# Kernel optimization log

Measured on AMD Instinct MI355X. Metric: run time of the kernel, lower is better.

Reference implementation:

```python
import jax, jax.numpy as jnp
import numpy as np

N_NODES = 100000
N_EDGES = 1600000
IN_NODE = 64
IN_EDGE = 16
HID = 128
OUT = 128
N_CONVS = 3
NEG_SLOPE = 0.01  # LeakyReLU default
LN_EPS = 1e-5


def setup_inputs() -> dict:
    key = jax.random.key(0)
    ks = jax.random.split(key, 16)
    x = jax.random.normal(ks[0], (N_NODES, IN_NODE), dtype=jnp.float32)
    edge_attr = jax.random.normal(ks[1], (N_EDGES, IN_EDGE), dtype=jnp.float32)
    edge_index = jax.random.randint(ks[2], (2, N_EDGES), 0, N_NODES, dtype=jnp.int64)
    # xavier-normal-ish init for linears
    def lin(k, fi, fo):
        return jax.random.normal(k, (fi, fo), dtype=jnp.float32) * jnp.sqrt(2.0 / (fi + fo))
    W_node = lin(ks[3], IN_NODE, HID)
    b_node = jnp.zeros((HID,), jnp.float32)
    W_edge = lin(ks[4], IN_EDGE, HID)
    b_edge = jnp.zeros((HID,), jnp.float32)
    W_conv = jax.random.normal(ks[5], (N_CONVS, HID, HID), dtype=jnp.float32) * jnp.sqrt(1.0 / HID)
    b_conv = jnp.zeros((N_CONVS, HID), jnp.float32)
    W_head = lin(ks[6], HID, OUT)
    b_head = jnp.zeros((OUT,), jnp.float32)
    ln_gamma = jnp.ones((OUT,), jnp.float32)
    ln_beta = jnp.zeros((OUT,), jnp.float32)
    return dict(x=x, edge_attr=edge_attr, edge_index=edge_index,
                W_node=W_node, b_node=b_node, W_edge=W_edge, b_edge=b_edge,
                W_conv=W_conv, b_conv=b_conv, W_head=W_head, b_head=b_head,
                ln_gamma=ln_gamma, ln_beta=ln_beta)


def _leaky_relu(x):
    return jnp.where(x >= 0, x, NEG_SLOPE * x)


def reference(x, edge_attr, edge_index, W_node, b_node, W_edge, b_edge,
              W_conv, b_conv, W_head, b_head, ln_gamma, ln_beta):
    src, dst = edge_index[0], edge_index[1]
    h = x @ W_node + b_node                  # [N, H]
    e = edge_attr @ W_edge + b_edge          # [E, H]
    skip = h
    for l in range(N_CONVS):
        # GINEConv (eps=0): nn((1+eps)*h_i + sum_j relu(h_j + e_ij)), nn = Linear + LeakyReLU
        msg = jax.nn.relu(h[src] + e)        # [E, H]
        agg = jax.ops.segment_sum(msg, dst, num_segments=N_NODES)  # [N, H]
        h = _leaky_relu((h + agg) @ W_conv[l] + b_conv[l])
    h = skip + h
    # head: Linear + LayerNorm
    y = h @ W_head + b_head                  # [N, OUT]
    mu = jnp.mean(y, axis=-1, keepdims=True)
    var = jnp.mean(jnp.square(y - mu), axis=-1, keepdims=True)
    return (y - mu) * jax.lax.rsqrt(var + LN_EPS) * ln_gamma + ln_beta
```

## Files before the change

### kernel.cpp

```cpp
#include <hip/hip_runtime.h>
#include <hip/hip_fp16.h>

constexpr int N      = 100000;
constexpr int E      = 1600000;
constexpr int F_IN   = 64;
constexpr int F_EDGE = 16;
constexpr int H      = 128;
constexpr int NB     = (N + 255) / 256;
constexpr float NEG  = 0.01f;
constexpr float EPS  = 1e-5f;

typedef _Float16 hv2 __attribute__((ext_vector_type(2)));

__global__ __launch_bounds__(256) void k_zero(int* __restrict__ p, int n) {
  int i = blockIdx.x * 256 + threadIdx.x;
  if (i < n) p[i] = 0;
}

__global__ __launch_bounds__(256) void k_hist(const int* __restrict__ eidx, int* __restrict__ deg) {
  int i = blockIdx.x * 256 + threadIdx.x;
  if (i < E) atomicAdd(&deg[eidx[E + i]], 1);
}

__global__ __launch_bounds__(256) void k_scan_block(const int* __restrict__ deg,
    int* __restrict__ excl, int* __restrict__ bsum) {
  __shared__ int s[256];
  int t = threadIdx.x, i = blockIdx.x * 256 + t;
  int v = (i < N) ? deg[i] : 0;
  s[t] = v; __syncthreads();
#pragma unroll
  for (int off = 1; off < 256; off <<= 1) {
    int u = (t >= off) ? s[t - off] : 0;
    __syncthreads();
    s[t] += u;
    __syncthreads();
  }
  if (i < N) excl[i] = s[t] - v;
  if (t == 255) bsum[blockIdx.x] = s[255];
}

__global__ __launch_bounds__(512) void k_scan_top(const int* __restrict__ bsum, int* __restrict__ boff) {
  __shared__ int s[512];
  int t = threadIdx.x;
  int v = (t < NB) ? bsum[t] : 0;
  s[t] = v; __syncthreads();
#pragma unroll
  for (int off = 1; off < 512; off <<= 1) {
    int u = (t >= off) ? s[t - off] : 0;
    __syncthreads();
    s[t] += u;
    __syncthreads();
  }
  if (t < NB) boff[t] = s[t] - v;
}

__global__ __launch_bounds__(256) void k_scan_add(const int* __restrict__ excl,
    const int* __restrict__ boff, int* __restrict__ rowptr, int* __restrict__ cursor) {
  int i = blockIdx.x * 256 + threadIdx.x;
  if (i < N) {
    int r = excl[i] + boff[i >> 8];
    rowptr[i] = r;
    cursor[i] = r;
  }
}

__global__ __launch_bounds__(256) void k_scatter(const int* __restrict__ eidx,
    const float* __restrict__ edge_attr, int* __restrict__ cursor,
    int* __restrict__ csr_src, uint4* __restrict__ csr_a16) {
  int i = blockIdx.x * 256 + threadIdx.x;
  if (i >= E) return;
  int d = eidx[E + i];
  int pos = atomicAdd(&cursor[d], 1);
  csr_src[pos] = eidx[i];
  const float4* ar = (const float4*)(edge_attr + (size_t)i * F_EDGE);
  float4 f0 = ar[0], f1 = ar[1], f2 = ar[2], f3 = ar[3];
  __half2 hh[8];
  hh[0] = __float22half2_rn(make_float2(f0.x, f0.y));
  hh[1] = __float22half2_rn(make_float2(f0.z, f0.w));
  hh[2] = __float22half2_rn(make_float2(f1.x, f1.y));
  hh[3] = __float22half2_rn(make_float2(f1.z, f1.w));
  hh[4] = __float22half2_rn(make_float2(f2.x, f2.y));
  hh[5] = __float22half2_rn(make_float2(f2.z, f2.w));
  hh[6] = __float22half2_rn(make_float2(f3.x, f3.y));
  hh[7] = __float22half2_rn(make_float2(f3.z, f3.w));
  const uint4* u = (const uint4*)hh;
  csr_a16[2 * (size_t)pos + 0] = u[0];
  csr_a16[2 * (size_t)pos + 1] = u[1];
}

__global__ __launch_bounds__(256) void k_node_linear(
    const float* __restrict__ x, const float* __restrict__ W,
    const float* __restrict__ b, float* __restrict__ h, __half* __restrict__ h16) {
  __shared__ float xs[32][F_IN];
  int i0 = blockIdx.x * 32;
  {
    const float4* s4 = (const float4*)(x + (size_t)i0 * F_IN);
    float4* t4 = (float4*)xs;
#pragma unroll
    for (int r = 0; r < 2; ++r) t4[threadIdx.x + 256 * r] = s4[threadIdx.x + 256 * r];
  }
  __syncthreads();
  int c0 = (threadIdx.x & 31) * 4;
  int n0 = (threadIdx.x >> 5) * 4;
  float4 bb = *(const float4*)(b + c0);
  float4 acc[4] = {bb, bb, bb, bb};
#pragma unroll 4
  for (int k = 0; k < F_IN; ++k) {
    float4 w4 = *(const float4*)(W + k * H + c0);
#pragma unroll
    for (int j = 0; j < 4; ++j) {
      float s = xs[n0 + j][k];
      acc[j].x = fmaf(s, w4.x, acc[j].x);
      acc[j].y = fmaf(s, w4.y, acc[j].y);
      acc[j].z = fmaf(s, w4.z, acc[j].z);
      acc[j].w = fmaf(s, w4.w, acc[j].w);
    }
  }
#pragma unroll
  for (int j = 0; j < 4; ++j) {
    size_t idx = (size_t)(i0 + n0 + j) * H + c0;
    *(float4*)(h + idx) = acc[j];
    __half2* ph = (__half2*)(h16 + idx);
    ph[0] = __float22half2_rn(make_float2(acc[j].x, acc[j].y));
    ph[1] = __float22half2_rn(make_float2(acc[j].z, acc[j].w));
  }
}

__device__ __forceinline__ void dot16(uint4 A0, uint4 A1,
                                      const hv2* __restrict__ wA, const hv2* __restrict__ wB,
                                      float& tx, float& ty) {
  unsigned u[8] = {A0.x, A0.y, A0.z, A0.w, A1.x, A1.y, A1.z, A1.w};
#pragma unroll
  for (int j = 0; j < 8; ++j) {
    hv2 a = __builtin_bit_cast(hv2, u[j]);
    tx = __builtin_amdgcn_fdot2(a, wA[j], tx, false);
    ty = __builtin_amdgcn_fdot2(a, wB[j], ty, false);
  }
}

__global__ __launch_bounds__(256) void k_gather(
    const int* __restrict__ rowptr, const int* __restrict__ deg,
    const int* __restrict__ csr_src, const uint4* __restrict__ csr_a16,
    const __half2* __restrict__ h16, const float* __restrict__ We,
    const float* __restrict__ be, const float* __restrict__ h,
    float* __restrict__ sum) {
  int lane = threadIdx.x & 63;
  int node = (blockIdx.x * 256 + threadIdx.x) >> 6;
  if (node >= N) return;
  int c0 = 2 * lane;
  hv2 wA[8], wB[8];
#pragma unroll
  for (int j = 0; j < 8; ++j) {
    hv2 a, bq;
    a[0]  = (_Float16)We[(2 * j) * H + c0];
    a[1]  = (_Float16)We[(2 * j + 1) * H + c0];
    bq[0] = (_Float16)We[(2 * j) * H + c0 + 1];
    bq[1] = (_Float16)We[(2 * j + 1) * H + c0 + 1];
    wA[j] = a; wB[j] = bq;
  }
  float2 bias = ((const float2*)be)[lane];
  float2 acc = ((const float2*)(h + (size_t)node * H))[lane];
  int p0 = rowptr[node];
  int pend = p0 + deg[node];
  int p = p0;
  for (; p + 2 <= pend; p += 2) {
    int s0 = csr_src[p];
    int s1 = csr_src[p + 1];
    __half2 g0 = h16[(size_t)s0 * 64 + lane];
    __half2 g1 = h16[(size_t)s1 * 64 + lane];
    uint4 A0 = csr_a16[2 * (size_t)p + 0];
    uint4 A1 = csr_a16[2 * (size_t)p + 1];
    uint4 B0 = csr_a16[2 * (size_t)p + 2];
    uint4 B1 = csr_a16[2 * (size_t)p + 3];
    float t0x = bias.x, t0y = bias.y;
    float t1x = bias.x, t1y = bias.y;
    dot16(A0, A1, wA, wB, t0x, t0y);
    dot16(B0, B1, wA, wB, t1x, t1y);
    float2 gf0 = __half22float2(g0);
    float2 gf1 = __half22float2(g1);
    acc.x += fmaxf(gf0.x + t0x, 0.f) + fmaxf(gf1.x + t1x, 0.f);
    acc.y += fmaxf(gf0.y + t0y, 0.f) + fmaxf(gf1.y + t1y, 0.f);
  }
  for (; p < pend; ++p) {
    int s = csr_src[p];
    __half2 g = h16[(size_t)s * 64 + lane];
    uint4 A0 = csr_a16[2 * (size_t)p + 0];
    uint4 A1 = csr_a16[2 * (size_t)p + 1];
    float tx = bias.x, ty = bias.y;
    dot16(A0, A1, wA, wB, tx, ty);
    float2 gf = __half22float2(g);
    acc.x += fmaxf(gf.x + tx, 0.f);
    acc.y += fmaxf(gf.y + ty, 0.f);
  }
  ((float2*)sum)[(size_t)node * 64 + lane] = acc;
}

__global__ __launch_bounds__(256) void k_node_update(
    const float* __restrict__ sum, const float* __restrict__ W,
    const float* __restrict__ b, float* __restrict__ hout, __half* __restrict__ h16) {
  __shared__ float t[32][H];
  int i0 = blockIdx.x * 32;
  {
    const float4* s4 = (const float4*)(sum + (size_t)i0 * H);
    float4* t4 = (float4*)t;
#pragma unroll
    for (int r = 0; r < 4; ++r) t4[threadIdx.x + 256 * r] = s4[threadIdx.x + 256 * r];
  }
  __syncthreads();
  int c0 = (threadIdx.x & 31) * 4;
  int n0 = (threadIdx.x >> 5) * 4;
  float4 bb = *(const float4*)(b + c0);
  float4 acc[4] = {bb, bb, bb, bb};
#pragma unroll 4
  for (int k = 0; k < H; ++k) {
    float4 w4 = *(const float4*)(W + k * H + c0);
#pragma unroll
    for (int j = 0; j < 4; ++j) {
      float s = t[n0 + j][k];
      acc[j].x = fmaf(s, w4.x, acc[j].x);
      acc[j].y = fmaf(s, w4.y, acc[j].y);
      acc[j].z = fmaf(s, w4.z, acc[j].z);
      acc[j].w = fmaf(s, w4.w, acc[j].w);
    }
  }
#pragma unroll
  for (int j = 0; j < 4; ++j) {
    float4 a = acc[j];
    a.x = a.x >= 0.f ? a.x : NEG * a.x;
    a.y = a.y >= 0.f ? a.y : NEG * a.y;
    a.z = a.z >= 0.f ? a.z : NEG * a.z;
    a.w = a.w >= 0.f ? a.w : NEG * a.w;
    size_t idx = (size_t)(i0 + n0 + j) * H + c0;
    *(float4*)(hout + idx) = a;
    __half2* ph = (__half2*)(h16 + idx);
    ph[0] = __float22half2_rn(make_float2(a.x, a.y));
    ph[1] = __float22half2_rn(make_float2(a.z, a.w));
  }
}

__global__ __launch_bounds__(256) void k_head(
    const float* __restrict__ x, const float* __restrict__ Wn,
    const float* __restrict__ bn, const float* __restrict__ hfin,
    const float* __restrict__ W, const float* __restrict__ b,
    const float* __restrict__ gamma, const float* __restrict__ beta,
    float* __restrict__ out) {
  __shared__ float xs[32][F_IN];
  __shared__ float t[32][H];
  int i0 = blockIdx.x * 32;
  {
    const float4* s4 = (const float4*)(x + (size_t)i0 * F_IN);
    float4* t4 = (float4*)xs;
#pragma unroll
    for (int r = 0; r < 2; ++r) t4[threadIdx.x + 256 * r] = s4[threadIdx.x + 256 * r];
  }
  __syncthreads();
  int c0 = (threadIdx.x & 31) * 4;
  int n0 = (threadIdx.x >> 5) * 4;
  {
    float4 bb = *(const float4*)(bn + c0);
    float4 acc[4] = {bb, bb, bb, bb};
#pragma unroll 4
    for (int k = 0; k < F_IN; ++k) {
      float4 w4 = *(const float4*)(Wn + k * H + c0);
#pragma unroll
      for (int j = 0; j < 4; ++j) {
        float s = xs[n0 + j][k];
        acc[j].x = fmaf(s, w4.x, acc[j].x);
        acc[j].y = fmaf(s, w4.y, acc[j].y);
        acc[j].z = fmaf(s, w4.z, acc[j].z);
        acc[j].w = fmaf(s, w4.w, acc[j].w);
      }
    }
#pragma unroll
    for (int j = 0; j < 4; ++j) {
      float4 hf = *(const float4*)(hfin + (size_t)(i0 + n0 + j) * H + c0);
      acc[j].x += hf.x; acc[j].y += hf.y; acc[j].z += hf.z; acc[j].w += hf.w;
      *(float4*)&t[n0 + j][c0] = acc[j];
    }
  }
  __syncthreads();
  float4 bh = *(const float4*)(b + c0);
  float4 acc[4] = {bh, bh, bh, bh};
#pragma unroll 4
  for (int k = 0; k < H; ++k) {
    float4 w4 = *(const float4*)(W + k * H + c0);
#pragma unroll
    for (int j = 0; j < 4; ++j) {
      float s = t[n0 + j][k];
      acc[j].x = fmaf(s, w4.x, acc[j].x);
      acc[j].y = fmaf(s, w4.y, acc[j].y);
      acc[j].z = fmaf(s, w4.z, acc[j].z);
      acc[j].w = fmaf(s, w4.w, acc[j].w);
    }
  }
  float4 g4 = *(const float4*)(gamma + c0);
  float4 b4 = *(const float4*)(beta + c0);
#pragma unroll
  for (int j = 0; j < 4; ++j) {
    float S  = acc[j].x + acc[j].y + acc[j].z + acc[j].w;
    float S2 = acc[j].x * acc[j].x + acc[j].y * acc[j].y
             + acc[j].z * acc[j].z + acc[j].w * acc[j].w;
#pragma unroll
    for (int off = 16; off > 0; off >>= 1) {
      S  += __shfl_down(S, off, 32);
      S2 += __shfl_down(S2, off, 32);
    }
    S  = __shfl(S, 0, 32);
    S2 = __shfl(S2, 0, 32);
    float mu  = S * (1.f / H);
    float var = S2 * (1.f / H) - mu * mu;
    float inv = rsqrtf(var + EPS);
    float4 o;
    o.x = (acc[j].x - mu) * inv * g4.x + b4.x;
    o.y = (acc[j].y - mu) * inv * g4.y + b4.y;
    o.z = (acc[j].z - mu) * inv * g4.z + b4.z;
    o.w = (acc[j].w - mu) * inv * g4.w + b4.w;
    *(float4*)(out + (size_t)(i0 + n0 + j) * H + c0) = o;
  }
}

extern "C" void kernel_launch(void* const* d_in, const int* in_sizes, int n_in,
                              void* d_out, int out_size, void* d_ws, size_t ws_size,
                              hipStream_t stream) {
  const float* x         = (const float*)d_in[0];
  const float* edge_attr = (const float*)d_in[1];
  const int*   eidx      = (const int*)d_in[2];
  const float* W_node    = (const float*)d_in[3];
  const float* b_node    = (const float*)d_in[4];
  const float* W_edge    = (const float*)d_in[5];
  const float* b_edge    = (const float*)d_in[6];
  const float* W_conv    = (const float*)d_in[7];
  const float* b_conv    = (const float*)d_in[8];
  const float* W_head    = (const float*)d_in[9];
  const float* b_head    = (const float*)d_in[10];
  const float* gamma     = (const float*)d_in[11];
  const float* beta      = (const float*)d_in[12];
  float* out = (float*)d_out;

  size_t S = (size_t)N * H;
  float*   h       = (float*)d_ws;
  uint4*   csr_a16 = (uint4*)(h + S);
  __half*  h16     = (__half*)(csr_a16 + 2 * (size_t)E);
  int*     csr_src = (int*)(h16 + S);
  int*     deg     = csr_src + E;
  int*     excl    = deg + N;
  int*     rowptr  = excl + N;
  int*     cursor  = rowptr + N;
  int*     bsum    = cursor + N;
  int*     boff    = bsum + 512;
  float*   sum     = out;

  const int eb = (E + 255) / 256;

  k_zero<<<NB, 256, 0, stream>>>(deg, N);
  k_hist<<<eb, 256, 0, stream>>>(eidx, deg);
  k_scan_block<<<NB, 256, 0, stream>>>(deg, excl, bsum);
  k_scan_top<<<1, 512, 0, stream>>>(bsum, boff);
  k_scan_add<<<NB, 256, 0, stream>>>(excl, boff, rowptr, cursor);
  k_scatter<<<eb, 256, 0, stream>>>(eidx, edge_attr, cursor, csr_src, csr_a16);

  k_node_linear<<<N / 32, 256, 0, stream>>>(x, W_node, b_node, h, h16);

  for (int l = 0; l < 3; ++l) {
    k_gather<<<N / 4, 256, 0, stream>>>(rowptr, deg, csr_src, csr_a16,
                                        (const __half2*)h16, W_edge, b_edge, h, sum);
    k_node_update<<<N / 32, 256, 0, stream>>>(
        sum, W_conv + (size_t)l * H * H, b_conv + (size_t)l * H, h, h16);
  }

  k_head<<<N / 32, 256, 0, stream>>>(x, W_node, b_node, h, W_head, b_head, gamma, beta, out);
}
```

Baseline: 1.183 ms.

## Drop fp32 node state in favor of fp16 and split CSR scatter into permute+pack

Node features h and the aggregated sum are now stored only in fp16 (h16, sum16), removing the fp32 h buffer and the fp32 sum round-trip between gather and node-update. This halves the bytes written and read per layer. The CSR build is split so that k_scatter only records a permutation, and a new k_pack kernel writes csr_src and the fp16 edge attributes with coalesced stores. The cost is an extra kernel launch, a perm buffer, and more rounding error from keeping the residual and aggregate in fp16.

After: 1.252 ms. 1.06x slower.

```diff
diff --git a/kernel.cpp b/kernel.cpp
--- a/kernel.cpp
+++ b/kernel.cpp
@@ -65,14 +65,22 @@
 }
 
 __global__ __launch_bounds__(256) void k_scatter(const int* __restrict__ eidx,
-    const float* __restrict__ edge_attr, int* __restrict__ cursor,
-    int* __restrict__ csr_src, uint4* __restrict__ csr_a16) {
+    int* __restrict__ cursor, int* __restrict__ perm) {
   int i = blockIdx.x * 256 + threadIdx.x;
   if (i >= E) return;
   int d = eidx[E + i];
   int pos = atomicAdd(&cursor[d], 1);
-  csr_src[pos] = eidx[i];
-  const float4* ar = (const float4*)(edge_attr + (size_t)i * F_EDGE);
+  perm[pos] = i;
+}
+
+__global__ __launch_bounds__(256) void k_pack(const int* __restrict__ perm,
+    const int* __restrict__ eidx, const float* __restrict__ edge_attr,
+    int* __restrict__ csr_src, uint4* __restrict__ csr_a16) {
+  int p = blockIdx.x * 256 + threadIdx.x;
+  if (p >= E) return;
+  int eid = perm[p];
+  csr_src[p] = eidx[eid];
+  const float4* ar = (const float4*)(edge_attr + (size_t)eid * F_EDGE);
   float4 f0 = ar[0], f1 = ar[1], f2 = ar[2], f3 = ar[3];
   __half2 hh[8];
   hh[0] = __float22half2_rn(make_float2(f0.x, f0.y));
@@ -84,13 +92,13 @@
   hh[6] = __float22half2_rn(make_float2(f3.x, f3.y));
   hh[7] = __float22half2_rn(make_float2(f3.z, f3.w));
   const uint4* u = (const uint4*)hh;
-  csr_a16[2 * (size_t)pos + 0] = u[0];
-  csr_a16[2 * (size_t)pos + 1] = u[1];
+  csr_a16[2 * (size_t)p + 0] = u[0];
+  csr_a16[2 * (size_t)p + 1] = u[1];
 }
 
 __global__ __launch_bounds__(256) void k_node_linear(
     const float* __restrict__ x, const float* __restrict__ W,
-    const float* __restrict__ b, float* __restrict__ h, __half* __restrict__ h16) {
+    const float* __restrict__ b, __half* __restrict__ h16) {
   __shared__ float xs[32][F_IN];
   int i0 = blockIdx.x * 32;
   {
@@ -118,9 +126,7 @@
   }
 #pragma unroll
   for (int j = 0; j < 4; ++j) {
-    size_t idx = (size_t)(i0 + n0 + j) * H + c0;
-    *(float4*)(h + idx) = acc[j];
-    __half2* ph = (__half2*)(h16 + idx);
+    __half2* ph = (__half2*)(h16 + (size_t)(i0 + n0 + j) * H + c0);
     ph[0] = __float22half2_rn(make_float2(acc[j].x, acc[j].y));
     ph[1] = __float22half2_rn(make_float2(acc[j].z, acc[j].w));
   }
@@ -142,8 +148,7 @@
     const int* __restrict__ rowptr, const int* __restrict__ deg,
     const int* __restrict__ csr_src, const uint4* __restrict__ csr_a16,
     const __half2* __restrict__ h16, const float* __restrict__ We,
-    const float* __restrict__ be, const float* __restrict__ h,
-    float* __restrict__ sum) {
+    const float* __restrict__ be, __half2* __restrict__ sum16) {
   int lane = threadIdx.x & 63;
   int node = (blockIdx.x * 256 + threadIdx.x) >> 6;
   if (node >= N) return;
@@ -159,7 +164,7 @@
     wA[j] = a; wB[j] = bq;
   }
   float2 bias = ((const float2*)be)[lane];
-  float2 acc = ((const float2*)(h + (size_t)node * H))[lane];
+  float2 acc = __half22float2(h16[(size_t)node * 64 + lane]);
   int p0 = rowptr[node];
   int pend = p0 + deg[node];
   int p = p0;
@@ -192,19 +197,29 @@
     acc.x += fmaxf(gf.x + tx, 0.f);
     acc.y += fmaxf(gf.y + ty, 0.f);
   }
-  ((float2*)sum)[(size_t)node * 64 + lane] = acc;
+  sum16[(size_t)node * 64 + lane] = __float22half2_rn(acc);
 }
 
 __global__ __launch_bounds__(256) void k_node_update(
-    const float* __restrict__ sum, const float* __restrict__ W,
-    const float* __restrict__ b, float* __restrict__ hout, __half* __restrict__ h16) {
+    const __half* __restrict__ sum16, const float* __restrict__ W,
+    const float* __restrict__ b, __half* __restrict__ h16) {
   __shared__ float t[32][H];
   int i0 = blockIdx.x * 32;
   {
-    const float4* s4 = (const float4*)(sum + (size_t)i0 * H);
-    float4* t4 = (float4*)t;
-#pragma unroll
-    for (int r = 0; r < 4; ++r) t4[threadIdx.x + 256 * r] = s4[threadIdx.x + 256 * r];
+    const uint4* s4 = (const uint4*)(sum16 + (size_t)i0 * H);
+    float* tf = (float*)t;
+#pragma unroll
+    for (int r = 0; r < 2; ++r) {
+      uint4 v = s4[threadIdx.x + 256 * r];
+      const __half2* hp = (const __half2*)&v;
+      int base = (threadIdx.x + 256 * r) * 8;
+#pragma unroll
+      for (int j = 0; j < 4; ++j) {
+        float2 f = __half22float2(hp[j]);
+        tf[base + 2 * j]     = f.x;
+        tf[base + 2 * j + 1] = f.y;
+      }
+    }
   }
   __syncthreads();
   int c0 = (threadIdx.x & 31) * 4;
@@ -230,9 +245,7 @@
     a.y = a.y >= 0.f ? a.y : NEG * a.y;
     a.z = a.z >= 0.f ? a.z : NEG * a.z;
     a.w = a.w >= 0.f ? a.w : NEG * a.w;
-    size_t idx = (size_t)(i0 + n0 + j) * H + c0;
-    *(float4*)(hout + idx) = a;
-    __half2* ph = (__half2*)(h16 + idx);
+    __half2* ph = (__half2*)(h16 + (size_t)(i0 + n0 + j) * H + c0);
     ph[0] = __float22half2_rn(make_float2(a.x, a.y));
     ph[1] = __float22half2_rn(make_float2(a.z, a.w));
   }
@@ -240,7 +253,7 @@
 
 __global__ __launch_bounds__(256) void k_head(
     const float* __restrict__ x, const float* __restrict__ Wn,
-    const float* __restrict__ bn, const float* __restrict__ hfin,
+    const float* __restrict__ bn, const __half* __restrict__ hfin,
     const float* __restrict__ W, const float* __restrict__ b,
     const float* __restrict__ gamma, const float* __restrict__ beta,
     float* __restrict__ out) {
@@ -273,8 +286,10 @@
     }
 #pragma unroll
     for (int j = 0; j < 4; ++j) {
-      float4 hf = *(const float4*)(hfin + (size_t)(i0 + n0 + j) * H + c0);
-      acc[j].x += hf.x; acc[j].y += hf.y; acc[j].z += hf.z; acc[j].w += hf.w;
+      const __half2* hp = (const __half2*)(hfin + (size_t)(i0 + n0 + j) * H + c0);
+      float2 h0 = __half22float2(hp[0]);
+      float2 h1 = __half22float2(hp[1]);
+      acc[j].x += h0.x; acc[j].y += h0.y; acc[j].z += h1.x; acc[j].w += h1.y;
       *(float4*)&t[n0 + j][c0] = acc[j];
     }
   }
@@ -338,17 +353,17 @@
   float* out = (float*)d_out;
 
   size_t S = (size_t)N * H;
-  float*   h       = (float*)d_ws;
-  uint4*   csr_a16 = (uint4*)(h + S);
+  uint4*   csr_a16 = (uint4*)d_ws;
   __half*  h16     = (__half*)(csr_a16 + 2 * (size_t)E);
-  int*     csr_src = (int*)(h16 + S);
-  int*     deg     = csr_src + E;
+  __half*  sum16   = h16 + S;
+  int*     csr_src = (int*)(sum16 + S);
+  int*     perm    = csr_src + E;
+  int*     deg     = perm + E;
   int*     excl    = deg + N;
   int*     rowptr  = excl + N;
   int*     cursor  = rowptr + N;
   int*     bsum    = cursor + N;
   int*     boff    = bsum + 512;
-  float*   sum     = out;
 
   const int eb = (E + 255) / 256;
 
@@ -357,16 +372,18 @@
   k_scan_block<<<NB, 256, 0, stream>>>(deg, excl, bsum);
   k_scan_top<<<1, 512, 0, stream>>>(bsum, boff);
   k_scan_add<<<NB, 256, 0, stream>>>(excl, boff, rowptr, cursor);
-  k_scatter<<<eb, 256, 0, stream>>>(eidx, edge_attr, cursor, csr_src, csr_a16);
-
-  k_node_linear<<<N / 32, 256, 0, stream>>>(x, W_node, b_node, h, h16);
+  k_scatter<<<eb, 256, 0, stream>>>(eidx, cursor, perm);
+  k_pack<<<eb, 256, 0, stream>>>(perm, eidx, edge_attr, csr_src, csr_a16);
+
+  k_node_linear<<<N / 32, 256, 0, stream>>>(x, W_node, b_node, h16);
 
   for (int l = 0; l < 3; ++l) {
     k_gather<<<N / 4, 256, 0, stream>>>(rowptr, deg, csr_src, csr_a16,
-                                        (const __half2*)h16, W_edge, b_edge, h, sum);
+                                        (const __half2*)h16, W_edge, b_edge,
+                                        (__half2*)sum16);
     k_node_update<<<N / 32, 256, 0, stream>>>(
-        sum, W_conv + (size_t)l * H * H, b_conv + (size_t)l * H, h, h16);
-  }
-
-  k_head<<<N / 32, 256, 0, stream>>>(x, W_node, b_node, h, W_head, b_head, gamma, beta, out);
-}
+        sum16, W_conv + (size_t)l * H * H, b_conv + (size_t)l * H, h16);
+  }
+
+  k_head<<<N / 32, 256, 0, stream>>>(x, W_node, b_node, h16, W_head, b_head, gamma, beta, out);
+}
```
